# Optimization experiments

Measured on AMD Instinct MI355X. Metric: run time of the kernel, lower is better.

## Reference

```python
import jax, jax.numpy as jnp
import numpy as np

D = H = W = 64
N = D * H * W
BS = 2
C = 32          # enc_dim
IN_DIM = 4
OUT_DIM = 4
P = 5           # pos_enc_dim
COND = 32
M = 8           # modes per axis
NL = 4          # n_layers
NODE_IN = IN_DIM + 3 + 2 * P * 3   # 37
ENC_T = 1 + 2 * P                  # 11
ENC_C = ENC_T * COND               # 352
DT = 0.05


def fourier_embedding(pos, n_freq):
    # F(x) = [cos(2^i*pi*x_l), sin(2^i*pi*x_l)] per coordinate l, then concat x
    freq = (2.0 ** jnp.arange(n_freq, dtype=jnp.float32)) * jnp.pi  # (P,)
    ang = pos[..., None] * freq                                     # (..., L, P)
    emb = jnp.concatenate([jnp.cos(ang), jnp.sin(ang)], axis=-1)    # (..., L, 2P)
    emb = emb.reshape(*pos.shape[:-1], -1)                          # (..., L*2P)
    return jnp.concatenate([emb, pos], axis=-1)


def setup_inputs() -> dict:
    key = jax.random.key(0)
    ks = jax.random.split(key, 24)
    scale = 1.0 / C ** 2
    inp = {
        "state_in": jax.random.normal(ks[0], (BS, N, IN_DIM), jnp.float32),
        "node_pos": jax.random.uniform(ks[1], (BS, N, 3), jnp.float32),
        "edges": jax.random.randint(ks[2], (BS, 16, 2), 0, N),
        "time_i": jax.random.uniform(ks[3], (BS, 1), jnp.float32),
        "conditions": jax.random.uniform(ks[4], (BS, COND), jnp.float32),
        "t_embed_w": jax.random.normal(ks[5], (C, ENC_T), jnp.float32) * 0.05,
        "t_embed_b": jax.random.normal(ks[6], (C,), jnp.float32) * 0.05,
        "c_embed_w": jax.random.normal(ks[7], (C, ENC_C), jnp.float32) * 0.05,
        "c_embed_b": jax.random.normal(ks[8], (C,), jnp.float32) * 0.05,
        "lift_w": jax.random.normal(ks[9], (C, NODE_IN), jnp.float32) * 0.05,
        "lift_b": jax.random.normal(ks[10], (C,), jnp.float32) * 0.05,
        "spec_wr": jax.random.uniform(ks[11], (NL, C, C, M, M, M), jnp.float32) * scale,
        "spec_wi": jax.random.uniform(ks[12], (NL, C, C, M, M, M), jnp.float32) * scale,
        "byp_w": jax.random.normal(ks[13], (NL, C, C), jnp.float32) * 0.05,
        "byp_b": jax.random.normal(ks[14], (NL, C), jnp.float32) * 0.05,
        "proj1_w": jax.random.normal(ks[15], (C, C), jnp.float32) * 0.05,
        "proj1_b": jax.random.normal(ks[16], (C,), jnp.float32) * 0.05,
        "proj2_w": jax.random.normal(ks[17], (OUT_DIM, C), jnp.float32) * 0.05,
        "proj2_b": jax.random.normal(ks[18], (OUT_DIM,), jnp.float32) * 0.05,
    }
    return inp


def _conv1x1(x, w, b):
    # x: (b, c, d, h, w), w: (o, c), b: (o,)
    return jnp.einsum('bcdhw,oc->bodhw', x, w) + b[None, :, None, None, None]


def _fno_forward(state_in, node_pos, time_i, conditions,
                 t_embed_w, t_embed_b, c_embed_w, c_embed_b, lift_w, lift_b,
                 spec_wr, spec_wi, byp_w, byp_b, proj1_w, proj1_b, proj2_w, proj2_b):
    pos_enc = fourier_embedding(node_pos, P)      # (bs, N, 33)
    c_enc = fourier_embedding(conditions, P)      # (bs, 352)
    t_enc = fourier_embedding(time_i, P)          # (bs, 11)

    node_feat = jnp.concatenate([state_in, pos_enc], axis=-1)  # (bs, N, 37)
    t_emb = (t_enc @ t_embed_w.T + t_embed_b)[:, :, None, None, None]
    c_emb = (c_enc @ c_embed_w.T + c_embed_b)[:, :, None, None, None]

    # (bs, N, 37) -> (bs, 37, D, H, W)
    x = node_feat.transpose(0, 2, 1).reshape(BS, NODE_IN, D, H, W)
    x = _conv1x1(x, lift_w, lift_b)
    x = x + t_emb + c_emb

    for l in range(NL):
        w = jax.lax.complex(spec_wr[l], spec_wi[l])              # (C, C, M, M, M)
        x_ft = jnp.fft.rfftn(x, axes=(-3, -2, -1))               # (bs, C, D, H, W//2+1)
        blk = jnp.einsum('bixyz,ioxyz->boxyz', x_ft[..., :M, :M, :M], w)
        out_ft = jnp.zeros_like(x_ft).at[..., :M, :M, :M].set(blk)
        sp = jnp.fft.irfftn(out_ft, s=(D, H, W), axes=(-3, -2, -1))
        bp = _conv1x1(x, byp_w[l], byp_b[l])
        x = jax.nn.gelu(sp + bp, approximate=False)

    x = jax.nn.gelu(_conv1x1(x, proj1_w, proj1_b), approximate=False)
    x = _conv1x1(x, proj2_w, proj2_b)                            # (bs, 4, D, H, W)
    v_pred = x.reshape(BS, OUT_DIM, N).transpose(0, 2, 1)        # (bs, N, 4)
    return state_in + DT * v_pred


def reference(state_in, node_pos, edges, time_i, conditions,
              t_embed_w, t_embed_b, c_embed_w, c_embed_b, lift_w, lift_b,
              spec_wr, spec_wi, byp_w, byp_b, proj1_w, proj1_b, proj2_w, proj2_b):
    # edges are unused in the FNO forward (kept for API compatibility)
    return _fno_forward(state_in, node_pos, time_i, conditions,
                        t_embed_w, t_embed_b, c_embed_w, c_embed_b, lift_w, lift_b,
                        spec_wr, spec_wi, byp_w, byp_b, proj1_w, proj1_b, proj2_w, proj2_b)
```

## Files before the change

kernel.cpp:

```cpp
#include <hip/hip_runtime.h>
#include <math.h>

#define PI_F 3.14159265358979323846f

typedef __bf16 bf16x8 __attribute__((ext_vector_type(8)));
typedef float floatx4 __attribute__((ext_vector_type(4)));
union U8 { unsigned short u[8]; uint4 q; bf16x8 v; };

__device__ __forceinline__ float gelu_fast(float v) {
    float v2 = v * v;
    float u = 0.7978845608028654f * v * fmaf(0.044715f, v2, 1.0f);
    float a = fminf(fmaxf(u * 2.8853900817779268f, -30.0f), 30.0f);
    float e = __builtin_amdgcn_exp2f(a);
    float r = __builtin_amdgcn_rcpf(e + 1.0f);
    float th = fmaf(-2.0f, r, 1.0f);
    return 0.5f * v * (1.0f + th);
}
__device__ __forceinline__ int rfl(int x) { return __builtin_amdgcn_readfirstlane(x); }

__device__ __forceinline__ unsigned short f2bf(float f) {
    unsigned int u = __float_as_uint(f);
    u += 0x7fffu + ((u >> 16) & 1u);
    return (unsigned short)(u >> 16);
}
__device__ __forceinline__ float bf2f(unsigned short h) {
    return __uint_as_float(((unsigned int)h) << 16);
}

__device__ __forceinline__ void swz8k(int blk, int& b, int& nx, int& ny) {
    int x = blk & 7;
    int j = blk >> 3;
    int pair = x * 16 + (j >> 6);
    ny = j & 63;
    b = pair >> 6;
    nx = pair & 63;
}

__global__ void k_emb(const float* __restrict__ time_i, const float* __restrict__ conditions,
                      const float* __restrict__ t_embed_w, const float* __restrict__ t_embed_b,
                      const float* __restrict__ c_embed_w, const float* __restrict__ c_embed_b,
                      const float* __restrict__ lift_b, float* __restrict__ embk) {
    __shared__ float red[8][32];
    int t = threadIdx.x;
    int b = blockIdx.x;
    int c = t & 31, lg = t >> 5;
    float acc = 0.0f;
    if (lg == 0) {
        acc = t_embed_b[c] + c_embed_b[c] + lift_b[c];
        float tv = time_i[b];
        float ang = PI_F * tv;
        const float* tw = t_embed_w + c * 11;
        for (int i = 0; i < 5; i++) {
            float s, co; sincosf(ang, &s, &co);
            acc += co * tw[i] + s * tw[5 + i];
            ang *= 2.0f;
        }
        acc += tv * tw[10];
    }
    const float* cw = c_embed_w + c * 352;
    for (int j = 0; j < 4; j++) {
        int l = lg * 4 + j;
        float v = conditions[b * 32 + l];
        float ang = PI_F * v;
        for (int i = 0; i < 5; i++) {
            float s, co; sincosf(ang, &s, &co);
            acc += co * cw[l * 10 + i] + s * cw[l * 10 + 5 + i];
            ang *= 2.0f;
        }
        acc += v * cw[320 + l];
    }
    red[lg][c] = acc;
    __syncthreads();
    if (t < 32) {
        float s = 0.0f;
        for (int g = 0; g < 8; g++) s += red[g][t];
        embk[b * 32 + t] = s;
    }
}

__global__ void k_wt(const float* __restrict__ byp_w, const float* __restrict__ lift_w,
                     unsigned short* __restrict__ wbh, unsigned short* __restrict__ wlbf,
                     unsigned short* __restrict__ Tinv, unsigned short* __restrict__ TfT) {
    int idx = blockIdx.x * 256 + threadIdx.x;
    const float th = PI_F / 32.0f;
    if (idx < 4096) {
        wbh[idx] = f2bf(byp_w[idx]);
    } else if (idx < 6144) {
        int j = idx - 4096;
        int o = j >> 6, q = j & 63;
        wlbf[j] = (q < 37) ? f2bf(lift_w[o * 37 + q]) : 0;
    } else if (idx < 8192) {
        int j = idx - 6144;
        int nz = j >> 5, k = j & 31;
        int kz = k >> 1;
        float val = 0.0f;
        if (kz < 8) {
            float a = (float)((kz * nz) & 63) * th;
            val = (k & 1) ? sinf(a) : cosf(a);
        }
        Tinv[j] = f2bf(val);
    } else if (idx < 9216) {
        int j = idx - 8192;
        int kcol = j >> 6, nz = j & 63;
        int kz = kcol >> 1;
        float a = (float)((kz * nz) & 63) * th;
        float val = (kcol & 1) ? -sinf(a) : cosf(a);
        TfT[j] = f2bf(val);
    }
}

__global__ __launch_bounds__(256) void k_lift(const float* __restrict__ state_in,
        const float* __restrict__ node_pos, const unsigned short* __restrict__ wlbf,
        const float* __restrict__ embk, const unsigned short* __restrict__ TfT,
        unsigned short* __restrict__ x0, float2* __restrict__ a1) {
    __shared__ __align__(16) float SL[7584];
    unsigned short* fsT  = (unsigned short*)SL;
    unsigned short* ysbf = (unsigned short*)(SL + 2304);
    float* pz   = SL + 3456;
    float* bias = SL + 7552;
    int t = threadIdx.x;
    int b, nx, ny; swz8k(blockIdx.x, b, nx, ny);
    int nxy = nx * 64 + ny;

    if (t < 32) bias[t] = embk[b * 32 + t];
    {
        for (int u = t; u < 2048; u += 256) {
            int row = u >> 5, col = 37 + (u & 31);
            fsT[row * 72 + col] = 0;
        }
    }
    if (t < 192) {
        int nzf = t / 3;
        int l = t - nzf * 3;
        float p = node_pos[((size_t)b * 262144 + (nxy << 6)) * 3 + t];
        float s, c; sincosf(PI_F * p, &s, &c);
        unsigned short* row = fsT + nzf * 72;
        #pragma unroll
        for (int i = 0; i < 5; i++) {
            row[4 + l * 10 + i] = f2bf(c);
            row[4 + l * 10 + 5 + i] = f2bf(s);
            float nc = 2.0f * c * c - 1.0f;
            s = 2.0f * s * c;
            c = nc;
        }
        row[34 + l] = f2bf(p);
    } else {
        int nzf = t - 192;
        const float4 s4 = *(const float4*)(state_in + ((size_t)b * 262144 + (nxy << 6) + nzf) * 4);
        unsigned short* row = fsT + nzf * 72;
        row[0] = f2bf(s4.x); row[1] = f2bf(s4.y);
        row[2] = f2bf(s4.z); row[3] = f2bf(s4.w);
    }
    __syncthreads();

    int lane = t & 63;
    int w = rfl(t >> 6);
    int otile = w & 1;
    int nzt0 = (w >> 1) * 2;
    int l15 = lane & 15;
    int quad = lane >> 4;

    U8 a0, a1_;
    a0.q = *(const uint4*)(wlbf + ((otile * 16 + l15) << 6) + (quad << 3));
    a1_.q = *(const uint4*)(wlbf + ((otile * 16 + l15) << 6) + 32 + (quad << 3));
    floatx4 dz = {0.0f, 0.0f, 0.0f, 0.0f};

    #pragma unroll
    for (int m = 0; m < 2; m++) {
        int nzc = (nzt0 + m) * 16 + l15;
        U8 b0, b1_;
        b0.q = *(const uint4*)(fsT + nzc * 72 + (quad << 3));
        b1_.q = *(const uint4*)(fsT + nzc * 72 + 32 + (quad << 3));
        floatx4 d = __builtin_amdgcn_mfma_f32_16x16x32_bf16(a0.v, b0.v, dz, 0, 0, 0);
        d = __builtin_amdgcn_mfma_f32_16x16x32_bf16(a1_.v, b1_.v, d, 0, 0, 0);
        #pragma unroll
        for (int r = 0; r < 4; r++) {
            int o = otile * 16 + quad * 4 + r;
            float v = d[r] + bias[o];
            unsigned short hv = f2bf(v);
            x0[(((size_t)(b * 32 + o)) << 18) + (nxy << 6) + nzc] = hv;
            ysbf[o * 72 + nzc] = hv;
        }
    }
    __syncthreads();
    {
        int khalf = w >> 1;
        U8 ay, bt;
        ay.q = *(const uint4*)(ysbf + (otile * 16 + l15) * 72 + khalf * 32 + (quad << 3));
        bt.q = *(const uint4*)(TfT + (l15 << 6) + khalf * 32 + (quad << 3));
        floatx4 d = __builtin_amdgcn_mfma_f32_16x16x32_bf16(ay.v, bt.v, dz, 0, 0, 0);
        *(floatx4*)(pz + w * 1024 + lane * 4) = d;
    }
    __syncthreads();
    if (w < 2) {
        float4 p0 = *(float4*)(pz + w * 1024 + lane * 4);
        float4 p1 = *(float4*)(pz + (w + 2) * 1024 + lane * 4);
        float* a1f = (float*)a1 + ((size_t)(b * 4096 + nxy)) * 512;
        #pragma unroll
        for (int r = 0; r < 4; r++) {
            int o = otile * 16 + quad * 4 + r;
            float pv[4] = {p0.x + p1.x, p0.y + p1.y, p0.z + p1.z, p0.w + p1.w};
            a1f[(o << 4) + l15] = pv[r];
        }
    }
}


__global__ __launch_bounds__(256) void k_p1(const float2* __restrict__ a1,
                                            float2* __restrict__ a2p) {
    int blk = blockIdx.x, t = threadIdx.x;
    int x = blk & 7, r = blk >> 3;
    int pair = x * 16 + (r & 15);
    int half = r >> 4;
    const float2* src = a1 + ((size_t)(pair * 64 + half * 32)) * 256 + t;
    float accr[8], acci[8];
    #pragma unroll
    for (int k = 0; k < 8; k++) { accr[k] = 0.0f; acci[k] = 0.0f; }
    const float bc = 0.99518472667f;
    const float bs = -0.09801714033f;
    float wc = half ? -1.0f : 1.0f;
    float ws = 0.0f;
    #pragma unroll 4
    for (int j = 0; j < 32; j++) {
        float2 v = src[(size_t)j * 256];
        accr[0] += v.x; acci[0] += v.y;
        float tc = wc, ts = ws;
        #pragma unroll
        for (int ky = 1; ky < 8; ky++) {
            accr[ky] += v.x * tc - v.y * ts;
            acci[ky] += v.x * ts + v.y * tc;
            float nt = tc * wc - ts * ws; ts = ts * wc + tc * ws; tc = nt;
        }
        float nw = wc * bc - ws * bs; ws = ws * bc + wc * bs; wc = nw;
    }
    float4* dst = (float4*)(a2p + (size_t)half * 262144 + ((size_t)(pair * 256 + t)) * 8);
    #pragma unroll
    for (int j = 0; j < 4; j++)
        dst[j] = make_float4(accr[2 * j], acci[2 * j], accr[2 * j + 1], acci[2 * j + 1]);
}

__global__ __launch_bounds__(256) void k_p2(const float2* __restrict__ a2p,
                                            float2* __restrict__ xft) {
    __shared__ __align__(16) float2 SH[1040];
    int blk = blockIdx.x, t = threadIdx.x;
    for (int lu = 0; lu < 2; lu++) {
        int un = blk * 2 + lu;
        int b = un >> 8, ckz = un & 255;
        size_t base = (size_t)b * 131072 + (size_t)ckz * 8;
        for (int e = t; e < 512; e += 256) {
            size_t a = base + (size_t)(e >> 3) * 2048 + (e & 7);
            float2 v0 = a2p[a];
            float2 v1 = a2p[a + 262144];
            SH[lu * 520 + e] = make_float2(v0.x + v1.x, v0.y + v1.y);
        }
    }
    __syncthreads();
    if (t < 128) {
        int lu = t >> 6, out = t & 63;
        int un = blk * 2 + lu;
        int kx = out & 7;
        float sn, cc; sincosf((float)kx * (PI_F / 32.0f), &sn, &cc);
        float bsn = -sn;
        float tc = 1.0f, ts = 0.0f, rr = 0.0f, ri = 0.0f;
        const float2* row = SH + lu * 520 + (out >> 3);
        for (int nx = 0; nx < 64; nx++) {
            float2 v = row[nx * 8];
            rr += v.x * tc - v.y * ts;
            ri += v.x * ts + v.y * tc;
            float nt = tc * cc - ts * bsn; ts = ts * cc + tc * bsn; tc = nt;
        }
        xft[(size_t)un * 64 + out] = make_float2(rr, ri);
    }
}

__global__ __launch_bounds__(256) void k_p3(const float2* __restrict__ xft,
        const float* __restrict__ wr, const float* __restrict__ wi,
        float2* __restrict__ yftp) {
    __shared__ __align__(16) float2 SH[128];
    int blk = blockIdx.x, t = threadIdx.x;
    int unit = blk >> 1, ih = blk & 1;
    int b = unit >> 6, kx = (unit >> 3) & 7, ky = unit & 7;
    if (t < 128) {
        int il = t >> 3, kz = t & 7;
        int i = ih * 16 + il;
        SH[t] = xft[((size_t)((b * 32 + i) * 8 + kz)) * 64 + ky * 8 + kx];
    }
    __syncthreads();
    int o = t >> 3, kz = t & 7;
    float yr = 0.0f, yi = 0.0f;
    for (int il = 0; il < 16; il++) {
        int i = ih * 16 + il;
        float2 xv = SH[il * 8 + kz];
        int wofs = ((i * 32 + o) << 9) + kx * 64 + ky * 8 + kz;
        float wrv = wr[wofs], wiv = wi[wofs];
        yr += xv.x * wrv - xv.y * wiv;
        yi += xv.x * wiv + xv.y * wrv;
    }
    yftp[(size_t)ih * 32768 + ((size_t)((b * 32 + o) * 8 + kz)) * 64 + ky * 8 + kx]
        = make_float2(yr, yi);
}

__global__ __launch_bounds__(256) void k_p4(const float2* __restrict__ yftp,
                                            float2* __restrict__ b1) {
    __shared__ __align__(16) float2 SH[4608];
    int blk = blockIdx.x, t = threadIdx.x;
    for (int u = 0; u < 2; u++) {
        if (u) __syncthreads();
        int unit = blk * 2 + u;
        int b = unit >> 8, nx = (unit >> 2) & 63, og = unit & 3;
        size_t sbase = ((size_t)(b * 32 + og * 8)) * 512;
        for (int e = t; e < 4096; e += 256) {
            float2 v0 = yftp[sbase + e];
            float2 v1 = yftp[32768 + sbase + e];
            SH[(e >> 3) * 9 + (e & 7)] = make_float2(v0.x + v1.x, v0.y + v1.y);
        }
        __syncthreads();
        float cs, ss; sincosf((float)nx * (PI_F / 32.0f), &ss, &cs);
        float2* dst = b1 + ((size_t)(b * 64 + nx)) * 2048 + og * 512;
        for (int h = 0; h < 2; h++) {
            int idx = h * 256 + t;
            const float2* row = SH + idx * 9;
            float c = 1.0f, s = 0.0f, rr = 0.0f, ri = 0.0f;
            #pragma unroll
            for (int kx = 0; kx < 8; kx++) {
                float2 y = row[kx];
                rr += y.x * c - y.y * s;
                ri += y.x * s + y.y * c;
                float nc = c * cs - s * ss; s = s * cs + c * ss; c = nc;
            }
            dst[idx] = make_float2(rr, ri);
        }
    }
}

__global__ __launch_bounds__(256) void k_fin(
        const unsigned short* __restrict__ xin, const float2* __restrict__ b1,
        const unsigned short* __restrict__ wbh, const float* __restrict__ bb,
        const unsigned short* __restrict__ Tinv, const unsigned short* __restrict__ TfT,
        unsigned short* __restrict__ xout, float2* __restrict__ a1, int do_z,
        int do_proj, const float* __restrict__ state_in, const float* __restrict__ p1w,
        const float* __restrict__ p1b, const float* __restrict__ p2w,
        const float* __restrict__ p2b, float* __restrict__ outp) {
    __shared__ __align__(16) float S[7232];
    float* b1sr = S;
    float* b1si = S + 2112;
    float* pz   = S;
    float* pr   = S;
    unsigned short* xsu  = (unsigned short*)(S + 4224);
    unsigned short* msbf = (unsigned short*)(S + 5280);
    unsigned short* ysbf = (unsigned short*)(S + 5920);
    float* cosT = S + 7072;
    float* sinT = S + 7136;
    float* bias = S + 7200;
    int t = threadIdx.x;
    int b, nx, ny; swz8k(blockIdx.x, b, nx, ny);
    int nxy = nx * 64 + ny;

    if (t < 64) { float s, c; sincosf((float)t * (PI_F / 32.0f), &s, &c); cosT[t] = c; sinT[t] = s; }
    if (t >= 96 && t < 128) bias[t - 96] = bb[t - 96];
    ((unsigned int*)msbf)[(t >> 3) * 20 + 8 + (t & 7)] = 0;
    {
        int ch = t >> 3, q = t & 7;
        uint4 v = *(const uint4*)(xin + (((size_t)b) << 23) + (nxy << 6)
                                  + ((size_t)ch << 18) + q * 8);
        unsigned int* dst = (unsigned int*)(xsu + ch * 66 + q * 8);
        dst[0] = v.x; dst[1] = v.y; dst[2] = v.z; dst[3] = v.w;
    }
    const float2* bsrc = b1 + ((size_t)(b * 64 + nx)) * 2048;
    for (int u = 0; u < 8; u++) {
        int g = u * 256 + t;
        float2 v = bsrc[g];
        int ky = g & 7, okz = g >> 3;
        b1sr[ky * 264 + okz] = v.x;
        b1si[ky * 264 + okz] = v.y;
    }
    __syncthreads();
    const float scale = 1.0f / 262144.0f;
    {
        float mr = 0.0f, mi = 0.0f;
        #pragma unroll
        for (int ky = 0; ky < 8; ky++) {
            float vr = b1sr[ky * 264 + t], vi = b1si[ky * 264 + t];
            int m_ = (ky * ny) & 63;
            float c = cosT[m_], s = sinT[m_];
            mr += vr * c - vi * s;
            mi += vr * s + vi * c;
        }
        int kz = t & 7;
        float sc = (kz == 0) ? scale : 2.0f * scale;
        unsigned int pk = (unsigned int)f2bf(mr * sc)
                        | ((unsigned int)f2bf(-mi * sc) << 16);
        ((unsigned int*)msbf)[(t >> 3) * 20 + kz] = pk;
    }
    __syncthreads();

    int lane = t & 63;
    int w = rfl(t >> 6);
    int otile = w & 1;
    int nzt0 = (w >> 1) * 2;
    int l15 = lane & 15;
    int quad = lane >> 4;

    U8 aw, ams;
    aw.q = *(const uint4*)(wbh + ((otile * 16 + l15) << 5) + (quad << 3));
    ams.q = *(const uint4*)(msbf + (otile * 16 + l15) * 40 + (quad << 3));

    size_t colbase = (((size_t)b) << 23) + (nxy << 6);
    floatx4 dzero = {0.0f, 0.0f, 0.0f, 0.0f};

    #pragma unroll
    for (int m = 0; m < 2; m++) {
        int nzc = (nzt0 + m) * 16 + l15;
        U8 bx, bt;
        #pragma unroll
        for (int j = 0; j < 8; j++) bx.u[j] = xsu[(quad * 8 + j) * 66 + nzc];
        bt.q = *(const uint4*)(Tinv + (nzc << 5) + (quad << 3));
        floatx4 d = __builtin_amdgcn_mfma_f32_16x16x32_bf16(aw.v, bx.v, dzero, 0, 0, 0);
        d = __builtin_amdgcn_mfma_f32_16x16x32_bf16(ams.v, bt.v, d, 0, 0, 0);
        #pragma unroll
        for (int r = 0; r < 4; r++) {
            int o = otile * 16 + quad * 4 + r;
            float gv = gelu_fast(d[r] + bias[o]);
            unsigned short hv = f2bf(gv);
            if (!do_proj) xout[colbase + ((size_t)o << 18) + nzc] = hv;
            ysbf[o * 72 + nzc] = hv;
        }
    }

    if (do_z) {
        __syncthreads();
        int khalf = w >> 1;
        U8 ay, bt;
        ay.q = *(const uint4*)(ysbf + (otile * 16 + l15) * 72 + khalf * 32 + (quad << 3));
        bt.q = *(const uint4*)(TfT + (l15 << 6) + khalf * 32 + (quad << 3));
        floatx4 d = __builtin_amdgcn_mfma_f32_16x16x32_bf16(ay.v, bt.v, dzero, 0, 0, 0);
        *(floatx4*)(pz + w * 1024 + lane * 4) = d;
        __syncthreads();
        if (w < 2) {
            float4 p0 = *(float4*)(pz + w * 1024 + lane * 4);
            float4 p1 = *(float4*)(pz + (w + 2) * 1024 + lane * 4);
            float* a1f = (float*)a1 + ((size_t)(b * 4096 + nxy)) * 512;
            float pv[4] = {p0.x + p1.x, p0.y + p1.y, p0.z + p1.z, p0.w + p1.w};
            #pragma unroll
            for (int r = 0; r < 4; r++) {
                int o = otile * 16 + quad * 4 + r;
                a1f[(o << 4) + l15] = pv[r];
            }
        }
    }

    if (do_proj) {
        __syncthreads();
        int nz = t & 63;
        float xv[32];
        #pragma unroll
        for (int i = 0; i < 32; i++) xv[i] = bf2f(ysbf[i * 72 + nz]);
        float r0 = 0.f, r1 = 0.f, r2 = 0.f, r3 = 0.f;
        #pragma unroll
        for (int k = 0; k < 8; k++) {
            int o = w * 8 + k;
            float a = p1b[o];
            const float* wr = p1w + o * 32;
            #pragma unroll
            for (int i = 0; i < 32; i++) a += wr[i] * xv[i];
            float h = gelu_fast(a);
            r0 += p2w[0 * 32 + o] * h;
            r1 += p2w[1 * 32 + o] * h;
            r2 += p2w[2 * 32 + o] * h;
            r3 += p2w[3 * 32 + o] * h;
        }
        *(float4*)(pr + w * 256 + nz * 4) = make_float4(r0, r1, r2, r3);
        __syncthreads();
        if (t < 64) {
            float4 a0 = *(float4*)(pr + 0 * 256 + t * 4);
            float4 a1_ = *(float4*)(pr + 1 * 256 + t * 4);
            float4 a2 = *(float4*)(pr + 2 * 256 + t * 4);
            float4 a3 = *(float4*)(pr + 3 * 256 + t * 4);
            size_t base = ((size_t)b * 262144 + (nxy << 6) + t) * 4;
            float4 sv = *(const float4*)(state_in + base);
            *(float4*)(outp + base) = make_float4(
                sv.x + 0.05f * (p2b[0] + a0.x + a1_.x + a2.x + a3.x),
                sv.y + 0.05f * (p2b[1] + a0.y + a1_.y + a2.y + a3.y),
                sv.z + 0.05f * (p2b[2] + a0.z + a1_.z + a2.z + a3.z),
                sv.w + 0.05f * (p2b[3] + a0.w + a1_.w + a2.w + a3.w));
        }
    }
}

extern "C" void kernel_launch(void* const* d_in, const int* in_sizes, int n_in,
                              void* d_out, int out_size, void* d_ws, size_t ws_size,
                              hipStream_t stream) {
    const float* state_in   = (const float*)d_in[0];
    const float* node_pos   = (const float*)d_in[1];
    const float* time_i     = (const float*)d_in[3];
    const float* conditions = (const float*)d_in[4];
    const float* t_embed_w  = (const float*)d_in[5];
    const float* t_embed_b  = (const float*)d_in[6];
    const float* c_embed_w  = (const float*)d_in[7];
    const float* c_embed_b  = (const float*)d_in[8];
    const float* lift_w     = (const float*)d_in[9];
    const float* lift_b     = (const float*)d_in[10];
    const float* spec_wr    = (const float*)d_in[11];
    const float* spec_wi    = (const float*)d_in[12];
    const float* byp_w      = (const float*)d_in[13];
    const float* byp_b      = (const float*)d_in[14];
    const float* proj1_w    = (const float*)d_in[15];
    const float* proj1_b    = (const float*)d_in[16];
    const float* proj2_w    = (const float*)d_in[17];
    const float* proj2_b    = (const float*)d_in[18];
    float* out = (float*)d_out;
    float* ws  = (float*)d_ws;

    unsigned short* xA = (unsigned short*)ws;
    unsigned short* xB = (unsigned short*)(ws + 8388608);
    float2* a1   = (float2*)(ws + 16777216);
    float2* a2p  = (float2*)(ws + 20971520);
    float2* xft  = (float2*)(ws + 22020096);
    float2* yftp = (float2*)(ws + 22085632);
    float2* b1   = (float2*)(ws + 22216704);
    float*  embk = ws + 22740992;
    unsigned short* wbh  = (unsigned short*)(ws + 22741056);
    unsigned short* wlbf = (unsigned short*)(ws + 22743104);
    unsigned short* Tinv = (unsigned short*)(ws + 22744128);
    unsigned short* TfT  = (unsigned short*)(ws + 22745152);

    k_emb<<<2, 256, 0, stream>>>(time_i, conditions, t_embed_w, t_embed_b,
                                 c_embed_w, c_embed_b, lift_b, embk);
    k_wt<<<36, 256, 0, stream>>>(byp_w, lift_w, wbh, wlbf, Tinv, TfT);
    k_lift<<<8192, 256, 0, stream>>>(state_in, node_pos, wlbf, embk, TfT, xA, a1);

    for (int l = 0; l < 4; l++) {
        unsigned short* xin  = (l & 1) ? xB : xA;
        unsigned short* xout = (l & 1) ? xA : xB;
        const float* wrl = spec_wr + (size_t)l * 524288;
        const float* wil = spec_wi + (size_t)l * 524288;
        k_p1<<<256, 256, 0, stream>>>(a1, a2p);
        k_p2<<<256, 256, 0, stream>>>(a2p, xft);
        k_p3<<<256, 256, 0, stream>>>(xft, wrl, wil, yftp);
        k_p4<<<256, 256, 0, stream>>>(yftp, b1);
        k_fin<<<8192, 256, 0, stream>>>(xin, b1, wbh + l * 1024, byp_b + l * 32,
                                        Tinv, TfT, xout, a1, (l < 3) ? 1 : 0,
                                        (l == 3) ? 1 : 0, state_in,
                                        proj1_w, proj1_b, proj2_w, proj2_b, out);
    }
}
```

Baseline: 375.7 us.

## Stage outputs through LDS for vectorized stores, fold bias into MFMA, sigmoid GELU

```diff
diff --git a/kernel.cpp b/kernel.cpp
--- a/kernel.cpp
+++ b/kernel.cpp
@@ -7,14 +7,9 @@
 typedef float floatx4 __attribute__((ext_vector_type(4)));
 union U8 { unsigned short u[8]; uint4 q; bf16x8 v; };
 
-__device__ __forceinline__ float gelu_fast(float v) {
-    float v2 = v * v;
-    float u = 0.7978845608028654f * v * fmaf(0.044715f, v2, 1.0f);
-    float a = fminf(fmaxf(u * 2.8853900817779268f, -30.0f), 30.0f);
-    float e = __builtin_amdgcn_exp2f(a);
-    float r = __builtin_amdgcn_rcpf(e + 1.0f);
-    float th = fmaf(-2.0f, r, 1.0f);
-    return 0.5f * v * (1.0f + th);
+__device__ __forceinline__ float gelu_sig(float v) {
+    float e = __builtin_amdgcn_exp2f(-2.4554670f * v);
+    return v * __builtin_amdgcn_rcpf(1.0f + e);
 }
 __device__ __forceinline__ int rfl(int x) { return __builtin_amdgcn_readfirstlane(x); }
 
@@ -117,6 +112,7 @@
     unsigned short* fsT  = (unsigned short*)SL;
     unsigned short* ysbf = (unsigned short*)(SL + 2304);
     float* pz   = SL + 3456;
+    float* pz2  = SL + 3456 + 512;
     float* bias = SL + 7552;
     int t = threadIdx.x;
     int b, nx, ny; swz8k(blockIdx.x, b, nx, ny);
@@ -163,6 +159,9 @@
     U8 a0, a1_;
     a0.q = *(const uint4*)(wlbf + ((otile * 16 + l15) << 6) + (quad << 3));
     a1_.q = *(const uint4*)(wlbf + ((otile * 16 + l15) << 6) + 32 + (quad << 3));
+    floatx4 cb;
+    #pragma unroll
+    for (int r = 0; r < 4; r++) cb[r] = bias[otile * 16 + quad * 4 + r];
     floatx4 dz = {0.0f, 0.0f, 0.0f, 0.0f};
 
     #pragma unroll
@@ -171,18 +170,20 @@
         U8 b0, b1_;
         b0.q = *(const uint4*)(fsT + nzc * 72 + (quad << 3));
         b1_.q = *(const uint4*)(fsT + nzc * 72 + 32 + (quad << 3));
-        floatx4 d = __builtin_amdgcn_mfma_f32_16x16x32_bf16(a0.v, b0.v, dz, 0, 0, 0);
+        floatx4 d = __builtin_amdgcn_mfma_f32_16x16x32_bf16(a0.v, b0.v, cb, 0, 0, 0);
         d = __builtin_amdgcn_mfma_f32_16x16x32_bf16(a1_.v, b1_.v, d, 0, 0, 0);
         #pragma unroll
         for (int r = 0; r < 4; r++) {
             int o = otile * 16 + quad * 4 + r;
-            float v = d[r] + bias[o];
-            unsigned short hv = f2bf(v);
-            x0[(((size_t)(b * 32 + o)) << 18) + (nxy << 6) + nzc] = hv;
-            ysbf[o * 72 + nzc] = hv;
-        }
-    }
-    __syncthreads();
+            ysbf[o * 72 + nzc] = f2bf(d[r]);
+        }
+    }
+    __syncthreads();
+    {
+        int ch = t >> 3, q = t & 7;
+        uint4 v = *(const uint4*)(ysbf + ch * 72 + q * 8);
+        *(uint4*)(x0 + (((size_t)(b * 32 + ch)) << 18) + (nxy << 6) + q * 8) = v;
+    }
     {
         int khalf = w >> 1;
         U8 ay, bt;
@@ -195,13 +196,16 @@
     if (w < 2) {
         float4 p0 = *(float4*)(pz + w * 1024 + lane * 4);
         float4 p1 = *(float4*)(pz + (w + 2) * 1024 + lane * 4);
+        float pv[4] = {p0.x + p1.x, p0.y + p1.y, p0.z + p1.z, p0.w + p1.w};
+        #pragma unroll
+        for (int r = 0; r < 4; r++)
+            pz2[(otile * 16 + quad * 4 + r) * 16 + l15] = pv[r];
+    }
+    __syncthreads();
+    if (t < 128) {
+        float4 v = *(float4*)(pz2 + t * 4);
         float* a1f = (float*)a1 + ((size_t)(b * 4096 + nxy)) * 512;
-        #pragma unroll
-        for (int r = 0; r < 4; r++) {
-            int o = otile * 16 + quad * 4 + r;
-            float pv[4] = {p0.x + p1.x, p0.y + p1.y, p0.z + p1.z, p0.w + p1.w};
-            a1f[(o << 4) + l15] = pv[r];
-        }
+        *(float4*)(a1f + t * 4) = v;
     }
 }
 
@@ -345,6 +349,7 @@
     float* b1sr = S;
     float* b1si = S + 2112;
     float* pz   = S;
+    float* pz2  = S + 512;
     float* pr   = S;
     unsigned short* xsu  = (unsigned short*)(S + 4224);
     unsigned short* msbf = (unsigned short*)(S + 5280);
@@ -404,9 +409,12 @@
     U8 aw, ams;
     aw.q = *(const uint4*)(wbh + ((otile * 16 + l15) << 5) + (quad << 3));
     ams.q = *(const uint4*)(msbf + (otile * 16 + l15) * 40 + (quad << 3));
+    floatx4 cb;
+    #pragma unroll
+    for (int r = 0; r < 4; r++) cb[r] = bias[otile * 16 + quad * 4 + r];
+    floatx4 dzero = {0.0f, 0.0f, 0.0f, 0.0f};
 
     size_t colbase = (((size_t)b) << 23) + (nxy << 6);
-    floatx4 dzero = {0.0f, 0.0f, 0.0f, 0.0f};
 
     #pragma unroll
     for (int m = 0; m < 2; m++) {
@@ -415,20 +423,23 @@
         #pragma unroll
         for (int j = 0; j < 8; j++) bx.u[j] = xsu[(quad * 8 + j) * 66 + nzc];
         bt.q = *(const uint4*)(Tinv + (nzc << 5) + (quad << 3));
-        floatx4 d = __builtin_amdgcn_mfma_f32_16x16x32_bf16(aw.v, bx.v, dzero, 0, 0, 0);
+        floatx4 d = __builtin_amdgcn_mfma_f32_16x16x32_bf16(aw.v, bx.v, cb, 0, 0, 0);
         d = __builtin_amdgcn_mfma_f32_16x16x32_bf16(ams.v, bt.v, d, 0, 0, 0);
         #pragma unroll
         for (int r = 0; r < 4; r++) {
             int o = otile * 16 + quad * 4 + r;
-            float gv = gelu_fast(d[r] + bias[o]);
-            unsigned short hv = f2bf(gv);
-            if (!do_proj) xout[colbase + ((size_t)o << 18) + nzc] = hv;
-            ysbf[o * 72 + nzc] = hv;
-        }
+            ysbf[o * 72 + nzc] = f2bf(gelu_sig(d[r]));
+        }
+    }
+    __syncthreads();
+
+    if (!do_proj) {
+        int ch = t >> 3, q = t & 7;
+        uint4 v = *(const uint4*)(ysbf + ch * 72 + q * 8);
+        *(uint4*)(xout + colbase + ((size_t)ch << 18) + q * 8) = v;
     }
 
     if (do_z) {
-        __syncthreads();
         int khalf = w >> 1;
         U8 ay, bt;
         ay.q = *(const uint4*)(ysbf + (otile * 16 + l15) * 72 + khalf * 32 + (quad << 3));
@@ -439,18 +450,20 @@
         if (w < 2) {
             float4 p0 = *(float4*)(pz + w * 1024 + lane * 4);
             float4 p1 = *(float4*)(pz + (w + 2) * 1024 + lane * 4);
-            float* a1f = (float*)a1 + ((size_t)(b * 4096 + nxy)) * 512;
             float pv[4] = {p0.x + p1.x, p0.y + p1.y, p0.z + p1.z, p0.w + p1.w};
             #pragma unroll
-            for (int r = 0; r < 4; r++) {
-                int o = otile * 16 + quad * 4 + r;
-                a1f[(o << 4) + l15] = pv[r];
-            }
+            for (int r = 0; r < 4; r++)
+                pz2[(otile * 16 + quad * 4 + r) * 16 + l15] = pv[r];
+        }
+        __syncthreads();
+        if (t < 128) {
+            float4 v = *(float4*)(pz2 + t * 4);
+            float* a1f = (float*)a1 + ((size_t)(b * 4096 + nxy)) * 512;
+            *(float4*)(a1f + t * 4) = v;
         }
     }
 
     if (do_proj) {
-        __syncthreads();
         int nz = t & 63;
         float xv[32];
         #pragma unroll
@@ -463,7 +476,7 @@
             const float* wr = p1w + o * 32;
             #pragma unroll
             for (int i = 0; i < 32; i++) a += wr[i] * xv[i];
-            float h = gelu_fast(a);
+            float h = gelu_sig(a);
             r0 += p2w[0 * 32 + o] * h;
             r1 += p2w[1 * 32 + o] * h;
             r2 += p2w[2 * 32 + o] * h;
```

New measurement: 360.6 us. 4.0% less time.
